# Kernel tuning notes

Measured on AMD Instinct MI355X. Metric: run time of the kernel, lower is better.

The kernel has to match this reference:

```python
import jax, jax.numpy as jnp
import numpy as np

EPS = 1e-6
HIDDEN = 8
SCALE = 1.0 / HIDDEN ** 0.5


def l2_normalize(t, axis=-1, eps=EPS):
    return t * jax.lax.rsqrt(jnp.sum(jnp.square(t), axis=axis, keepdims=True) + eps)


def setup_inputs() -> dict:
    key = jax.random.key(0)
    ks = jax.random.split(key, 6)
    B, S, N, D_IN, D_OUT = 2, 4096, 8, 2048, 2048
    x = jax.random.normal(ks[0], (B, S, D_IN), dtype=jnp.float32)
    bax = jax.random.normal(ks[1], (B, S, N, D_OUT), dtype=jnp.float32)
    # Linear params (stored as [in, hidden] for x @ W + b)
    W_q = jax.random.normal(ks[2], (D_IN, HIDDEN), dtype=jnp.float32) / np.sqrt(D_IN)
    b_q = jax.random.normal(ks[3], (HIDDEN,), dtype=jnp.float32) * 0.01
    W_k = jax.random.normal(ks[4], (D_OUT, HIDDEN), dtype=jnp.float32) / np.sqrt(D_OUT)
    b_k = jax.random.normal(ks[5], (HIDDEN,), dtype=jnp.float32) * 0.01
    return {"x": x, "bax": bax, "W_q": W_q, "b_q": b_q, "W_k": W_k, "b_k": b_k}


def reference(x, bax, W_q, b_q, W_k, b_k):
    # L2 normalize over feature dim
    xn = l2_normalize(x)                     # [B, S, D_in]
    baxn = l2_normalize(bax)                 # [B, S, N, D_out]
    queries = xn @ W_q + b_q                 # [B, S, H]
    keys = baxn @ W_k + b_k                  # [B, S, N, H]
    # scores: contract hidden dim per (b, s) position
    scores = jnp.einsum('bsh,bsnh->bsn', queries, keys) * SCALE  # [B, S, N]
    attention = jax.nn.softmax(scores, axis=-1)
    return attention
```

## Files before the change

### kernel.cpp

```cpp
#include <hip/hip_runtime.h>
#include <cstdint>

#define SCALE_F 0.35355339059327373f
#define EPS_F 1e-6f

template <int CTRL>
__device__ __forceinline__ float dppf(float s) {
    return __int_as_float(__builtin_amdgcn_update_dpp(
        0, __float_as_int(s), CTRL, 0xF, 0xF, true));
}
template <int PAT>
__device__ __forceinline__ float swz(float s) {
    return __int_as_float(__builtin_amdgcn_ds_swizzle(__float_as_int(s), PAT));
}
__device__ __forceinline__ float bf32s(float x) {
    auto r = __builtin_amdgcn_permlane32_swap(__float_as_int(x), __float_as_int(x),
                                              false, false);
    return __int_as_float(r[0]) + __int_as_float(r[1]);
}
__device__ __forceinline__ float bf32m(float x) {
    auto r = __builtin_amdgcn_permlane32_swap(__float_as_int(x), __float_as_int(x),
                                              false, false);
    return fmaxf(__int_as_float(r[0]), __int_as_float(r[1]));
}
#define DPP_X1 0xB1
#define DPP_X2 0x4E
#define DPP_R8 0x128
#define DPP_HM 0x141
#define SWZ_X4  0x101F
#define SWZ_X16 0x401F

#define BARRIER() do { \
    asm volatile("s_waitcnt lgkmcnt(0)" ::: "memory"); \
    __builtin_amdgcn_s_barrier(); \
    asm volatile("" ::: "memory"); \
} while (0)

#define ROW_BODY(R, BUF, PREFETCH) do { \
    const float e0 = v[R].x, e1 = v[R].y, e2 = v[R].z, e3 = v[R].w; \
    PREFETCH; \
    ssv[R] = fmaf(e3, e3, fmaf(e2, e2, fmaf(e1, e1, e0 * e0))); \
    float pd[8]; \
    _Pragma("unroll") \
    for (int h = 0; h < 8; ++h) \
        pd[h] = fmaf(e3, wreg[24 + h], fmaf(e2, wreg[16 + h], \
                 fmaf(e1, wreg[8 + h], e0 * wreg[h]))); \
    float r1[4]; \
    _Pragma("unroll") \
    for (int i = 0; i < 4; ++i) { \
        float keep = (lane & 1) ? pd[i + 4] : pd[i]; \
        float send = (lane & 1) ? pd[i] : pd[i + 4]; \
        r1[i] = keep + dppf<DPP_X1>(send); \
    } \
    float r2[2]; \
    _Pragma("unroll") \
    for (int i = 0; i < 2; ++i) { \
        float keep = (lane & 2) ? r1[i + 2] : r1[i]; \
        float send = (lane & 2) ? r1[i] : r1[i + 2]; \
        r2[i] = keep + dppf<DPP_X2>(send); \
    } \
    { \
        float keep = (lane & 4) ? r2[1] : r2[0]; \
        float send = (lane & 4) ? r2[0] : r2[1]; \
        float dv = keep + swz<SWZ_X4>(send); \
        dv += dppf<DPP_R8>(dv); \
        dv += swz<SWZ_X16>(dv); \
        dv = bf32s(dv); \
        if (lane < 8) red[BUF][R][w][chan] = dv; \
    } \
} while (0)

#define SS_REDUCE(BUF) do { \
    float r1[4]; \
    _Pragma("unroll") \
    for (int i = 0; i < 4; ++i) { \
        float keep = (lane & 1) ? ssv[i + 4] : ssv[i]; \
        float send = (lane & 1) ? ssv[i] : ssv[i + 4]; \
        r1[i] = keep + dppf<DPP_X1>(send); \
    } \
    float r2[2]; \
    _Pragma("unroll") \
    for (int i = 0; i < 2; ++i) { \
        float keep = (lane & 2) ? r1[i + 2] : r1[i]; \
        float send = (lane & 2) ? r1[i] : r1[i + 2]; \
        r2[i] = keep + dppf<DPP_X2>(send); \
    } \
    float keep = (lane & 4) ? r2[1] : r2[0]; \
    float send = (lane & 4) ? r2[0] : r2[1]; \
    float sv = keep + swz<SWZ_X4>(send); \
    sv += dppf<DPP_R8>(sv); \
    sv += swz<SWZ_X16>(sv); \
    sv = bf32s(sv); \
    if (lane < 8) red[BUF][chan][w][8] = sv; \
} while (0)

__global__ __launch_bounds__(512, 4)
void router_kernel(const float* __restrict__ x, const float* __restrict__ bax,
                   const float* __restrict__ Wq, const float* __restrict__ bq,
                   const float* __restrict__ Wk, const float* __restrict__ bk,
                   float* __restrict__ out, int positions) {
    __shared__ float red[2][8][8][13];
    __shared__ float qls[16][8];

    const int t = threadIdx.x;
    const int w = t >> 6;
    const int lane = t & 63;
    const int chan = ((lane & 1) << 2) | (lane & 2) | ((lane & 4) >> 2);
    const long pmax = positions - 1;
    const long pb = (long)blockIdx.x * 16;

    const float4* x4 = (const float4*)x + t;
    const float4* b4 = (const float4*)bax + t;

    float wreg[32];
    {
        const float4* q4 = (const float4*)(Wq + 32 * t);
#pragma unroll
        for (int j = 0; j < 8; ++j) {
            float4 a = q4[j];
            wreg[4 * j + 0] = a.x; wreg[4 * j + 1] = a.y;
            wreg[4 * j + 2] = a.z; wreg[4 * j + 3] = a.w;
        }
    }
    const float bqh = bq[lane & 7];
    const float bkh = bk[lane & 7];

    float4 v[8];
    float ssv[8];

#pragma unroll
    for (int r = 0; r < 8; ++r) {
        long p = pb + r; if (p > pmax) p = pmax;
        v[r] = x4[p * 512];
    }

#pragma unroll
    for (int r = 0; r < 8; ++r) {
        long p = pb + 8 + r; if (p > pmax) p = pmax;
        ROW_BODY(r, 0, v[r] = x4[p * 512]);
    }
    SS_REDUCE(0);
    BARRIER();
    if (w == 0) {
        const int pr = lane >> 3, h = lane & 7;
        float dt = 0.f, ss = 0.f;
#pragma unroll
        for (int wv = 0; wv < 8; ++wv) {
            dt += red[0][pr][wv][h];
            ss += red[0][pr][wv][8];
        }
        qls[pr][h] = fmaf(dt, rsqrtf(ss + EPS_F), bqh);
    }

    {
        long p0 = pb; if (p0 > pmax) p0 = pmax;
#pragma unroll
        for (int r = 0; r < 8; ++r) {
            ROW_BODY(r, 1, v[r] = b4[(p0 * 8 + r) * 512]);
        }
    }
    SS_REDUCE(1);
    {
        const float4* k4 = (const float4*)(Wk + 32 * t);
#pragma unroll
        for (int j = 0; j < 8; ++j) {
            float4 a = k4[j];
            wreg[4 * j + 0] = a.x; wreg[4 * j + 1] = a.y;
            wreg[4 * j + 2] = a.z; wreg[4 * j + 3] = a.w;
        }
    }
    BARRIER();
    if (w == 0) {
        const int pr = lane >> 3, h = lane & 7;
        float dt = 0.f, ss = 0.f;
#pragma unroll
        for (int wv = 0; wv < 8; ++wv) {
            dt += red[1][pr][wv][h];
            ss += red[1][pr][wv][8];
        }
        qls[8 + pr][h] = fmaf(dt, rsqrtf(ss + EPS_F), bqh);
    }

#pragma unroll 1
    for (int j = 0; j < 16; ++j) {
        const int bf = j & 1;
        long p = pb + j; if (p > pmax) p = pmax;
        long pn = pb + j + 1; if (pn > pmax) pn = pmax;
        const bool pref = (j < 15);
#pragma unroll
        for (int r = 0; r < 8; ++r) {
            ROW_BODY(r, bf, if (pref) v[r] = b4[(pn * 8 + r) * 512]);
        }
        SS_REDUCE(bf);
        BARRIER();
        if (w == 0) {
            const int kn = lane >> 3, hh = lane & 7;
            float dtk = 0.f, ssk = 0.f;
#pragma unroll
            for (int wv = 0; wv < 8; ++wv) {
                dtk += red[bf][kn][wv][hh];
                ssk += red[bf][kn][wv][8];
            }
            float kval = fmaf(dtk, rsqrtf(ssk + EPS_F), bkh);
            float qv = qls[j][hh];
            float s = qv * kval;
            s += dppf<DPP_X1>(s);
            s += dppf<DPP_X2>(s);
            s += dppf<DPP_HM>(s);
            s *= SCALE_F;
            float mx = fmaxf(s, dppf<DPP_R8>(s));
            mx = fmaxf(mx, swz<SWZ_X16>(mx));
            mx = bf32m(mx);
            float ev = __expf(s - mx);
            float den = ev + dppf<DPP_R8>(ev);
            den += swz<SWZ_X16>(den);
            den = bf32s(den);
            if (hh == 0 && pb + j < positions) out[p * 8 + kn] = ev / den;
        }
    }
}

extern "C" void kernel_launch(void* const* d_in, const int* in_sizes, int n_in,
                              void* d_out, int out_size, void* d_ws, size_t ws_size,
                              hipStream_t stream) {
    const float* x   = (const float*)d_in[0];
    const float* bax = (const float*)d_in[1];
    const float* Wq  = (const float*)d_in[2];
    const float* bq  = (const float*)d_in[3];
    const float* Wk  = (const float*)d_in[4];
    const float* bk  = (const float*)d_in[5];
    float* out = (float*)d_out;

    const int positions = in_sizes[0] / 2048;
    const int nb = (positions + 15) / 16;
    router_kernel<<<nb, 512, 0, stream>>>(x, bax, Wq, bq, Wk, bk, out, positions);
}
```

Before: 114.4 us.

## Pre-permute weights per lane to drop shuffle selects and use packed FMAs

Adds a small pre-pass kernel that rearranges Wq and Wk into a workspace so each lane's weights are XOR-permuted by its lane index. The butterfly reduction can then skip the per-lane keep/send selects, and the projection uses 2-wide vector FMAs (packed fp32). This is meant to cut VALU instruction count in a kernel bound by bandwidth plus instruction issue. The cost is an extra kernel launch and a workspace dependency, and the reduction now lands results in permuted channel order.

```diff
diff --git a/kernel.cpp b/kernel.cpp
--- a/kernel.cpp
+++ b/kernel.cpp
@@ -3,6 +3,8 @@
 
 #define SCALE_F 0.35355339059327373f
 #define EPS_F 1e-6f
+
+typedef float v2f __attribute__((ext_vector_type(2)));
 
 template <int CTRL>
 __device__ __forceinline__ float dppf(float s) {
@@ -27,7 +29,6 @@
 #define DPP_X2 0x4E
 #define DPP_R8 0x128
 #define DPP_HM 0x141
-#define SWZ_X4  0x101F
 #define SWZ_X16 0x401F
 
 #define BARRIER() do { \
@@ -37,37 +38,31 @@
 } while (0)
 
 #define ROW_BODY(R, BUF, PREFETCH) do { \
-    const float e0 = v[R].x, e1 = v[R].y, e2 = v[R].z, e3 = v[R].w; \
+    const v2f e01 = {v[R].x, v[R].y}; \
+    const v2f e23 = {v[R].z, v[R].w}; \
     PREFETCH; \
-    ssv[R] = fmaf(e3, e3, fmaf(e2, e2, fmaf(e1, e1, e0 * e0))); \
-    float pd[8]; \
-    _Pragma("unroll") \
-    for (int h = 0; h < 8; ++h) \
-        pd[h] = fmaf(e3, wreg[24 + h], fmaf(e2, wreg[16 + h], \
-                 fmaf(e1, wreg[8 + h], e0 * wreg[h]))); \
+    { v2f sq = e01 * e01 + e23 * e23; ssv[R] = sq.x + sq.y; } \
+    v2f pd2[4]; \
+    _Pragma("unroll") \
+    for (int c = 0; c < 4; ++c) { \
+        pd2[c] = e01.x * wr2[c]; \
+        pd2[c] += e01.y * wr2[4 + c]; \
+        pd2[c] += e23.x * wr2[8 + c]; \
+        pd2[c] += e23.y * wr2[12 + c]; \
+    } \
     float r1[4]; \
     _Pragma("unroll") \
-    for (int i = 0; i < 4; ++i) { \
-        float keep = (lane & 1) ? pd[i + 4] : pd[i]; \
-        float send = (lane & 1) ? pd[i] : pd[i + 4]; \
-        r1[i] = keep + dppf<DPP_X1>(send); \
-    } \
+    for (int i = 0; i < 4; ++i) \
+        r1[i] = pd2[i >> 1][i & 1] + dppf<DPP_X1>(pd2[2 + (i >> 1)][i & 1]); \
     float r2[2]; \
     _Pragma("unroll") \
-    for (int i = 0; i < 2; ++i) { \
-        float keep = (lane & 2) ? r1[i + 2] : r1[i]; \
-        float send = (lane & 2) ? r1[i] : r1[i + 2]; \
-        r2[i] = keep + dppf<DPP_X2>(send); \
-    } \
-    { \
-        float keep = (lane & 4) ? r2[1] : r2[0]; \
-        float send = (lane & 4) ? r2[0] : r2[1]; \
-        float dv = keep + swz<SWZ_X4>(send); \
-        dv += dppf<DPP_R8>(dv); \
-        dv += swz<SWZ_X16>(dv); \
-        dv = bf32s(dv); \
-        if (lane < 8) red[BUF][R][w][chan] = dv; \
-    } \
+    for (int i = 0; i < 2; ++i) \
+        r2[i] = r1[i] + dppf<DPP_X2>(r1[i + 2]); \
+    float dv = r2[0] + dppf<DPP_HM>(r2[1]); \
+    dv += dppf<DPP_R8>(dv); \
+    dv += swz<SWZ_X16>(dv); \
+    dv = bf32s(dv); \
+    if (lane < 8) red[BUF][R][w][lane] = dv; \
 } while (0)
 
 #define SS_REDUCE(BUF) do { \
@@ -87,18 +82,33 @@
     } \
     float keep = (lane & 4) ? r2[1] : r2[0]; \
     float send = (lane & 4) ? r2[0] : r2[1]; \
-    float sv = keep + swz<SWZ_X4>(send); \
+    float sv = keep + swz<0x101F>(send); \
     sv += dppf<DPP_R8>(sv); \
     sv += swz<SWZ_X16>(sv); \
     sv = bf32s(sv); \
     if (lane < 8) red[BUF][chan][w][8] = sv; \
 } while (0)
 
+__global__ void permute_w_kernel(const float* __restrict__ Wq,
+                                 const float* __restrict__ Wk,
+                                 float* __restrict__ pw) {
+    const int idx = blockIdx.x * 256 + threadIdx.x;
+    const int m = idx >> 14;
+    const int t = (idx >> 5) & 511;
+    const int s = idx & 31;
+    const int j = s >> 3;
+    const int i = s & 7;
+    const int M[8] = {0, 7, 2, 5, 1, 6, 3, 4};
+    const int h = (t & 7) ^ M[i];
+    const float* src = m ? Wk : Wq;
+    pw[idx] = src[(4 * t + j) * 8 + h];
+}
+
 __global__ __launch_bounds__(512, 4)
 void router_kernel(const float* __restrict__ x, const float* __restrict__ bax,
-                   const float* __restrict__ Wq, const float* __restrict__ bq,
-                   const float* __restrict__ Wk, const float* __restrict__ bk,
-                   float* __restrict__ out, int positions) {
+                   const float* __restrict__ pw, const float* __restrict__ bq,
+                   const float* __restrict__ bk, float* __restrict__ out,
+                   int positions) {
     __shared__ float red[2][8][8][13];
     __shared__ float qls[16][8];
 
@@ -112,14 +122,14 @@
     const float4* x4 = (const float4*)x + t;
     const float4* b4 = (const float4*)bax + t;
 
-    float wreg[32];
+    v2f wr2[16];
     {
-        const float4* q4 = (const float4*)(Wq + 32 * t);
+        const float4* q4 = (const float4*)(pw + 32 * t);
 #pragma unroll
         for (int j = 0; j < 8; ++j) {
             float4 a = q4[j];
-            wreg[4 * j + 0] = a.x; wreg[4 * j + 1] = a.y;
-            wreg[4 * j + 2] = a.z; wreg[4 * j + 3] = a.w;
+            wr2[2 * j + 0] = (v2f){a.x, a.y};
+            wr2[2 * j + 1] = (v2f){a.z, a.w};
         }
     }
     const float bqh = bq[lane & 7];
@@ -161,12 +171,12 @@
     }
     SS_REDUCE(1);
     {
-        const float4* k4 = (const float4*)(Wk + 32 * t);
+        const float4* k4 = (const float4*)(pw + 16384 + 32 * t);
 #pragma unroll
         for (int j = 0; j < 8; ++j) {
             float4 a = k4[j];
-            wreg[4 * j + 0] = a.x; wreg[4 * j + 1] = a.y;
-            wreg[4 * j + 2] = a.z; wreg[4 * j + 3] = a.w;
+            wr2[2 * j + 0] = (v2f){a.x, a.y};
+            wr2[2 * j + 1] = (v2f){a.z, a.w};
         }
     }
     BARRIER();
@@ -230,8 +240,10 @@
     const float* Wk  = (const float*)d_in[4];
     const float* bk  = (const float*)d_in[5];
     float* out = (float*)d_out;
+    float* pw  = (float*)d_ws;
 
     const int positions = in_sizes[0] / 2048;
+    permute_w_kernel<<<128, 256, 0, stream>>>(Wq, Wk, pw);
     const int nb = (positions + 15) / 16;
-    router_kernel<<<nb, 512, 0, stream>>>(x, bax, Wq, bq, Wk, bk, out, positions);
-}
+    router_kernel<<<nb, 512, 0, stream>>>(x, bax, pw, bq, bk, out, positions);
+}
```

Result: slower. 117.6 us (+2.8%).
